# Performance work log

Hardware: AMD Instinct MI355X
Metric: run time of the kernel (lower is better)

Reference implementation:

```python
import jax, jax.numpy as jnp
import numpy as np

# dims
B, H, W = 2, 128, 256
MD = 34            # model_dim (last 2 channels = sin/cos lat)
LD = MD - 2        # learnable_dim = 32
NH, HD = 4, 8      # n_heads, head_dim
SH = 64            # shared_hidden (DISCO out channels)
K = 25             # number of DISCO basis functions (5x5 kernel_shape)
P = 7              # local stencil width (lat x lon support of geodesic basis)
R = P // 2
FF1, FF2 = 512, 256


def setup_inputs() -> dict:
    key = jax.random.key(0)
    ks = jax.random.split(key, 16)
    x = jax.random.normal(ks[0], (B, H, W, MD), dtype=jnp.float32)
    # latitude-dependent sparse geodesic basis values over a 7x7 stencil
    psi_val = jax.random.uniform(ks[1], (K, H, P * P), dtype=jnp.float32) * 0.1
    disco_w = jax.random.normal(ks[2], (SH, K), dtype=jnp.float32) * 0.1
    disco_b = jax.random.normal(ks[3], (SH,), dtype=jnp.float32) * 0.01
    # per-head MLP: shared_hidden -> 32 -> 1
    hw1 = jax.random.normal(ks[4], (NH, SH, 32), dtype=jnp.float32) * (1.0 / np.sqrt(SH))
    hb1 = jax.random.normal(ks[5], (NH, 32), dtype=jnp.float32) * 0.01
    hw2 = jax.random.normal(ks[6], (NH, 32, 1), dtype=jnp.float32) * (1.0 / np.sqrt(32))
    hb2 = jax.random.normal(ks[7], (NH, 1), dtype=jnp.float32) * 0.01
    # FFN: model_dim -> 512 -> 256 -> learnable_dim
    fw1 = jax.random.normal(ks[8], (MD, FF1), dtype=jnp.float32) * (1.0 / np.sqrt(MD))
    fw1 = fw1.at[-2:, :].set(0.0)  # matches ffn[0].weight[:, -2:] = 0 init
    fb1 = jax.random.normal(ks[9], (FF1,), dtype=jnp.float32) * 0.01
    fw2 = jax.random.normal(ks[10], (FF1, FF2), dtype=jnp.float32) * (1.0 / np.sqrt(FF1))
    fb2 = jax.random.normal(ks[11], (FF2,), dtype=jnp.float32) * 0.01
    fw3 = jax.random.normal(ks[12], (FF2, LD), dtype=jnp.float32) * (1.0 / np.sqrt(FF2))
    fb3 = jax.random.normal(ks[13], (LD,), dtype=jnp.float32) * 0.01
    return {"x": x, "psi_val": psi_val, "disco_w": disco_w, "disco_b": disco_b,
            "hw1": hw1, "hb1": hb1, "hw2": hw2, "hb2": hb2,
            "fw1": fw1, "fb1": fb1, "fw2": fw2, "fb2": fb2, "fw3": fw3, "fb3": fb3}


def _gelu(t):
    return jax.nn.gelu(t, approximate=False)  # torch nn.GELU default (erf)


def _disco_s2(xn, psi_val, disco_w, disco_b):
    """DISCO sparse-basis conv on single-channel maps.
    xn: (N, H, W). Basis values vary with output latitude, longitude is
    translation-invariant; support is a lat-clamped / lon-wrapped 7x7 stencil.
    Returns (N, SH, H, W)."""
    xp = jnp.pad(xn, ((0, 0), (R, R), (0, 0)), mode="edge")  # clamp at poles
    shifts = []
    for dlat in range(P):
        row = xp[:, dlat:dlat + H, :]
        for dlon in range(-R, R + 1):
            shifts.append(jnp.roll(row, -dlon, axis=2))  # wrap in longitude
    xs = jnp.stack(shifts, axis=1)  # (N, P*P, H, W)
    basis = jnp.einsum("khp,nphw->nkhw", psi_val, xs)       # basis aggregation
    return jnp.einsum("fk,nkhw->nfhw", disco_w, basis) + disco_b[None, :, None, None]


def reference(x, psi_val, disco_w, disco_b, hw1, hb1, hw2, hb2,
              fw1, fb1, fw2, fb2, fw3, fb3):
    x_learn = x[..., :LD]
    sin_cos = x[..., LD:]
    x_res = x_learn
    # (B,H,W,LD) -> (B*LD, H, W): each learnable channel is a 1-channel map
    xn = x_learn.transpose(0, 3, 1, 2).reshape(B * LD, H, W)
    d = _disco_s2(xn, psi_val, disco_w, disco_b)              # (B*LD, SH, H, W)
    d = d.reshape(B, LD, SH, H, W).transpose(0, 3, 4, 1, 2)    # (B,H,W,LD,SH)
    # per-head MLP over its head_dim slice (head index is outer in LD)
    d = d.reshape(B, H, W, NH, HD, SH)
    h = _gelu(jnp.einsum("bxynds,nso->bxyndo", d, hw1) + hb1[None, None, None, :, None, :])
    h = jnp.einsum("bxyndo,noe->bxynde", h, hw2) + hb2[None, None, None, :, None, :]
    x_learn = h[..., 0].reshape(B, H, W, LD)
    x_learn = x_learn + x_res                                  # use_residual
    x_full = jnp.concatenate([x_learn, sin_cos], axis=-1)
    x_res2 = x_learn
    t = _gelu(x_full @ fw1 + fb1)
    t = _gelu(t @ fw2 + fb2)
    t = t @ fw3 + fb3                                          # dropout p=0 -> id
    x_learn = t + x_res2
    return jnp.concatenate([x_learn, sin_cos], axis=-1)
```

## Files before the change

kernel.cpp:

```cpp
#include <hip/hip_runtime.h>
#include <math.h>


typedef __attribute__((ext_vector_type(8))) short bfrag;
typedef __attribute__((ext_vector_type(4))) float ffrag;
typedef __attribute__((ext_vector_type(4))) short short4v;

union bfi4 { int4 i; bfrag b; };

__device__ __forceinline__ float gelu_f(float v) {
  const float z = v * (2.3022077484f + 0.1029451564f * v * v);
  const float e = __builtin_amdgcn_exp2f(-z);
  return v * __builtin_amdgcn_rcpf(1.0f + e);
}

__device__ __forceinline__ short f2bf(float f) {
  union { float f; unsigned u; } v; v.f = f;
  unsigned r = (v.u + 0x7fffu + ((v.u >> 16) & 1u)) >> 16;
  return (short)r;
}

__device__ __forceinline__ short f2bf_fast(float f) {
  union { float f; unsigned u; } v; v.f = f;
  return (short)((v.u + 0x8000u) >> 16);
}

__device__ __forceinline__ float bf2f(short s) {
  union { float f; unsigned u; } v;
  v.u = ((unsigned)(unsigned short)s) << 16;
  return v.f;
}

template <int CTRL>
__device__ __forceinline__ float dpp_add(float v) {
  union { float f; int i; } s, t;
  s.f = v;
  t.i = __builtin_amdgcn_update_dpp(0, s.i, CTRL, 0xf, 0xf, true);
  return v + t.f;
}
__device__ __forceinline__ float reduce16(float v) {
  v = dpp_add<0xB1>(v);
  v = dpp_add<0x4E>(v);
  v = dpp_add<0x141>(v);
  v = dpp_add<0x140>(v);
  return v;
}

__device__ __forceinline__ void st4bf(short* p, float4 v) {
  short4v s;
  s[0] = f2bf(v.x); s[1] = f2bf(v.y); s[2] = f2bf(v.z); s[3] = f2bf(v.w);
  *(short4v*)p = s;
}

__global__ __launch_bounds__(256) void k01_prep(
    const float* __restrict__ psi, const float* __restrict__ dw,
    const float* __restrict__ db,
    const float* __restrict__ fw1, const float* __restrict__ fw2,
    const float* __restrict__ fw3, const float* __restrict__ hw1,
    const float* __restrict__ hb1,
    short* __restrict__ wcb, short* __restrict__ fw1s,
    short* __restrict__ fw2s, short* __restrict__ fw3s,
    float* __restrict__ hb1e) {
  __shared__ __align__(16) char sm[24832];
  const int bid = blockIdx.x;
  const int tid = threadIdx.x;

  if (bid < 512) {
    float* tileL = (float*)sm;
    float* hw1n  = (float*)(sm + 13312);
    short* tile2 = (short*)(sm + 21504);
    const int h = bid >> 2;
    const int n = bid & 3;
    const int lane = tid & 63;
    const int w = __builtin_amdgcn_readfirstlane(tid >> 6);

    for (int e = tid; e < 512; e += 256)
      ((float4*)hw1n)[e] = ((const float4*)(hw1 + n * 2048))[e];

    float dwreg[25];
#pragma unroll
    for (int kk = 0; kk < 25; ++kk) dwreg[kk] = dw[lane * 25 + kk];
    const int p0 = w * 13;
    const int pend = (p0 + 13 < 49) ? (p0 + 13) : 49;
#pragma unroll 1
    for (int p = p0; p < pend; ++p) {
      float acc = 0.f;
#pragma unroll
      for (int kk = 0; kk < 25; ++kk)
        acc += dwreg[kk] * psi[kk * 6272 + h * 49 + p];
      tileL[lane * 52 + p] = acc;
    }
    __syncthreads();

    const int o = tid & 31;
#pragma unroll 1
    for (int pp = tid >> 5; pp < 25; pp += 8) {
      const int p2 = pp * 2;
      float a0 = 0.f, a1 = 0.f;
#pragma unroll 4
      for (int f = 0; f < 64; ++f) {
        const float wv = hw1n[f * 32 + o];
        a0 += wv * tileL[f * 52 + p2];
        a1 += wv * tileL[f * 52 + p2 + 1];
      }
      tile2[o * 52 + p2] = f2bf(a0);
      if (p2 + 1 < 49) tile2[o * 52 + p2 + 1] = f2bf(a1);
    }
    __syncthreads();

    short* outp = wcb + h * 16384 + n * 4096;
    for (int idx = tid; idx < 4096; idx += 256) {
      const int jj = idx & 7, ln = (idx >> 3) & 63;
      const int nt = (idx >> 9) & 1, kt = (idx >> 10) & 1;
      const int par = idx >> 11;
      const int k = kt * 32 + ((ln >> 4) << 3) + jj;
      const int oo = nt * 16 + (ln & 15);
      const int r = k >> 3, dlt = k & 7;
      const int j = par ? (dlt - 1) : dlt;
      short v = 0;
      if (r < 7 && j >= 0 && j < 7) v = tile2[oo * 52 + r * 7 + j];
      outp[idx] = v;
    }
    return;
  }

  if (bid < 528) {
    short* S = (short*)sm;
    const int kt = bid - 512;
    const float* src = fw2 + kt * 8192;
    for (int q = tid; q < 2048; q += 256) {
      const int lin = q * 4;
      const int kk = lin >> 8, nn = lin & 255;
      st4bf(S + kk * 260 + nn, *(const float4*)(src + lin));
    }
    __syncthreads();
    short* dst = fw2s + kt * 8192;
    for (int q = tid; q < 8192; q += 256) {
      const int jj = q & 7, lane = (q >> 3) & 63, nt = q >> 9;
      const int kk = (lane >> 4) * 8 + jj, nn = nt * 16 + (lane & 15);
      dst[q] = S[kk * 260 + nn];
    }
    return;
  }

  if (bid < 530) {
    const int X = bid - 528;
    short* S = (short*)sm;
    for (int q = tid; q < 2048; q += 256) {
      const int lin = q * 4;
      const int kk = lin >> 8, nn = lin & 255;
      st4bf(S + kk * 260 + nn, *(const float4*)(fw1 + kk * 512 + X * 256 + nn));
    }
    __syncthreads();
    for (int q = tid; q < 8192; q += 256) {
      const int jj = q & 7, lane = (q >> 3) & 63, ntl = q >> 9;
      const int kk = (lane >> 4) * 8 + jj, nn = ntl * 16 + (lane & 15);
      fw1s[X * 8192 + q] = S[kk * 260 + nn];
    }
    return;
  }

  if (bid == 530) {
    short* S = (short*)sm;
    for (int q = tid; q < 2048; q += 256) {
      const int lin = q * 4;
      const int kk = lin >> 5, nn = lin & 31;
      st4bf(S + kk * 36 + nn, *(const float4*)(fw3 + lin));
    }
    __syncthreads();
    for (int q = tid; q < 8192; q += 256) {
      const int jj = q & 7, lane = (q >> 3) & 63;
      const int nt = (q >> 9) & 1, kt = q >> 10;
      const int kk = kt * 32 + (lane >> 4) * 8 + jj, nn = nt * 16 + (lane & 15);
      fw3s[q] = S[kk * 36 + nn];
    }
    return;
  }

  if (tid < 128) {
    const int n = tid >> 5, o = tid & 31;
    float acc = hb1[n * 32 + o];
#pragma unroll
    for (int s = 0; s < 64; ++s)
      acc += hw1[n * 2048 + s * 32 + o] * db[s];
    hb1e[tid] = acc;
  }
}

__global__ __launch_bounds__(256, 7) void k23_fused(
    const float* __restrict__ x,    const short* __restrict__ wcb,
    const float* __restrict__ hb1e, const float* __restrict__ hw2,
    const float* __restrict__ hb2,
    const short* __restrict__ fw1s, const short* __restrict__ fw2s,
    const short* __restrict__ fw3s,
    const float* __restrict__ fb1,  const float* __restrict__ fb2,
    const float* __restrict__ fb3,  float* __restrict__ outb) {
  __shared__ __align__(16) char smem[20256];
  short* sX = (short*)smem;
  short* sM = (short*)(smem + 18080);
  float* sO = (float*)smem;

  const int tid = threadIdx.x;

  const int lin  = blockIdx.x + (blockIdx.y << 3) + (blockIdx.z << 10);
  const int xcd  = lin & 7;
  const int slot = lin >> 3;
  const int w0   = (slot & 7) * 32;
  const int b    = (slot >> 3) & 1;
  const int h    = (xcd << 4) | (slot >> 4);

  const int lane = tid & 63, lm = lane & 15, lq = lane >> 4;
  const int n = tid >> 6;

  float hb1v[2], hw2v[2];
#pragma unroll
  for (int nt = 0; nt < 2; ++nt) {
    hb1v[nt] = hb1e[n * 32 + nt * 16 + lm];
    hw2v[nt] = hw2[n * 32 + nt * 16 + lm];
  }
  const float hb2n = hb2[n];

  {
    int4* p = (int4*)smem;
    int4 z; z.x = z.y = z.z = z.w = 0;
    for (int e = tid; e < 20256 / 16; e += 256) p[e] = z;
  }
  __syncthreads();

#pragma unroll 1
  for (int r = 0; r < 7; ++r) {
    int hr = h - 3 + r; hr = hr < 0 ? 0 : (hr > 127 ? 127 : hr);
    const float* __restrict__ xrow = x + (size_t)((b * 128 + hr) * 256) * 34;
    short* __restrict__ sxr = sX + r * 40;
    for (int e = tid; e < 39 * 16; e += 256) {
      const int c2 = e & 15;
      const int wp = e >> 4;
      const int wr = (w0 - 3 + wp) & 255;
      const float2 v = *(const float2*)&xrow[wr * 34 + c2 * 2];
      short* dp = sxr + (c2 * 2) * 280 + wp;
      dp[0]   = f2bf_fast(v.x);
      dp[280] = f2bf_fast(v.y);
    }
  }
  __syncthreads();

  const int* tpB = (const int*)sX;

#pragma unroll 1
  for (int par = 0; par < 2; ++par) {
    bfrag cw[2][2];
#pragma unroll
    for (int kt = 0; kt < 2; ++kt)
#pragma unroll
      for (int nt = 0; nt < 2; ++nt)
        cw[kt][nt] = *(const bfrag*)(wcb + h * 16384 + n * 4096 +
                         ((par * 2 + kt) * 2 + nt) * 512 + lane * 8);

#pragma unroll 1
    for (int i = 0; i < 8; ++i) {
      const int c = n * 8 + i;

      const int base0 = c * 140 + lq * 20 + lm;
      bfi4 u0, u1;
      u0.i.x = tpB[base0];      u0.i.y = tpB[base0 + 1];
      u0.i.z = tpB[base0 + 2];  u0.i.w = tpB[base0 + 3];
      u1.i.x = tpB[base0 + 80]; u1.i.y = tpB[base0 + 81];
      u1.i.z = tpB[base0 + 82]; u1.i.w = tpB[base0 + 83];

      ffrag h0 = {0.f, 0.f, 0.f, 0.f}, h1 = {0.f, 0.f, 0.f, 0.f};
      h0 = __builtin_amdgcn_mfma_f32_16x16x32_bf16(u0.b, cw[0][0], h0, 0, 0, 0);
      h0 = __builtin_amdgcn_mfma_f32_16x16x32_bf16(u1.b, cw[1][0], h0, 0, 0, 0);
      h1 = __builtin_amdgcn_mfma_f32_16x16x32_bf16(u0.b, cw[0][1], h1, 0, 0, 0);
      h1 = __builtin_amdgcn_mfma_f32_16x16x32_bf16(u1.b, cw[1][1], h1, 0, 0, 0);

#pragma unroll
      for (int rr = 0; rr < 4; ++rr) {
        float v = gelu_f(h0[rr] + hb1v[0]) * hw2v[0] +
                  gelu_f(h1[rr] + hb1v[1]) * hw2v[1];
        v = reduce16(v);
        const int p = 2 * (lq * 4 + rr) + par;
        const float res = bf2f(sX[c * 280 + 123 + p]);
        if (lm == 0) sM[p * 34 + c] = f2bf_fast(v + hb2n + res);
      }
    }
  }
  __syncthreads();

  short* sT1h = (short*)smem;
  short* sT2  = (short*)smem;
  const int wave = n;
  const int koff = lq * 8;
  const int mt3 = wave & 1;
  const int nt3 = wave >> 1;
  const int col3 = nt3 * 16 + lm;
  const int pixg = (b * 128 + h) * 256 + w0;

  const int n0 = wave * 4;
  ffrag acc[2][4];
#pragma unroll
  for (int mt = 0; mt < 2; ++mt)
#pragma unroll
    for (int ni = 0; ni < 4; ++ni) acc[mt][ni] = ffrag{0.f, 0.f, 0.f, 0.f};
  const short* w2base = fw2s + n0 * 512 + lane * 8;

#pragma unroll 1
  for (int H = 0; H < 2; ++H) {
    bfrag aF[2];
#pragma unroll
    for (int mt = 0; mt < 2; ++mt)
      aF[mt] = *(const bfrag*)(sM + (mt * 16 + lm) * 34 + koff);
#pragma unroll
    for (int ni = 0; ni < 4; ++ni) {
      const bfrag b1f = *(const bfrag*)(fw1s +
                          (H * 16 + wave * 4 + ni) * 512 + lane * 8);
      const int ntl = wave * 4 + ni;
#pragma unroll
      for (int mt = 0; mt < 2; ++mt) {
        ffrag cc = {0.f, 0.f, 0.f, 0.f};
        cc = __builtin_amdgcn_mfma_f32_16x16x32_bf16(aF[mt], b1f, cc, 0, 0, 0);
        const int colg = H * 256 + ntl * 16 + lm;
        const float bias = fb1[colg];
#pragma unroll
        for (int r = 0; r < 4; ++r) {
          const int row = mt * 16 + lq * 4 + r;
          sT1h[row * 264 + ntl * 16 + lm] = f2bf_fast(gelu_f(cc[r] + bias));
        }
      }
    }
    __syncthreads();

#pragma unroll 2
    for (int kt = 0; kt < 8; ++kt) {
      bfrag bv[4];
#pragma unroll
      for (int ni = 0; ni < 4; ++ni)
        bv[ni] = *(const bfrag*)(w2base + (H * 8 + kt) * 8192 + ni * 512);
      const bfrag a0 = *(const bfrag*)(sT1h + lm * 264 + kt * 32 + koff);
      const bfrag a1 = *(const bfrag*)(sT1h + (16 + lm) * 264 + kt * 32 + koff);
#pragma unroll
      for (int ni = 0; ni < 4; ++ni) {
        acc[0][ni] = __builtin_amdgcn_mfma_f32_16x16x32_bf16(a0, bv[ni], acc[0][ni], 0, 0, 0);
        acc[1][ni] = __builtin_amdgcn_mfma_f32_16x16x32_bf16(a1, bv[ni], acc[1][ni], 0, 0, 0);
      }
    }
    __syncthreads();
  }

#pragma unroll
  for (int mt = 0; mt < 2; ++mt)
#pragma unroll
    for (int ni = 0; ni < 4; ++ni) {
      const int col = (n0 + ni) * 16 + lm;
      const float bias = fb2[col];
#pragma unroll
      for (int r = 0; r < 4; ++r) {
        const int row = mt * 16 + lq * 4 + r;
        sT2[row * 264 + col] = f2bf_fast(gelu_f(acc[mt][ni][r] + bias));
      }
    }
  __syncthreads();

  ffrag c3 = {0.f, 0.f, 0.f, 0.f};
  const short* sA3 = sT2 + (mt3 * 16 + lm) * 264 + koff;
#pragma unroll
  for (int kt = 0; kt < 8; ++kt) {
    const bfrag a = *(const bfrag*)(sA3 + kt * 32);
    const bfrag bw = *(const bfrag*)(fw3s + nt3 * 512 + kt * 1024 + lane * 8);
    c3 = __builtin_amdgcn_mfma_f32_16x16x32_bf16(a, bw, c3, 0, 0, 0);
  }
  __syncthreads();
  {
    const float bias = fb3[col3];
#pragma unroll
    for (int r = 0; r < 4; ++r) {
      const int row = mt3 * 16 + lq * 4 + r;
      const float res = bf2f(sM[(mt3 * 16 + lq * 4 + r) * 34 + col3]);
      sO[row * 34 + col3] = c3[r] + bias + res;
    }
  }
  if (tid < 32) {
    const float2 scv =
        *(const float2*)&x[(size_t)(((b * 128 + h) * 256 + w0 + tid)) * 34 + 32];
    sO[tid * 34 + 32] = scv.x;
    sO[tid * 34 + 33] = scv.y;
  }
  __syncthreads();
  {
    const float4* sp = (const float4*)sO;
    float4* dp = (float4*)(outb + (size_t)pixg * 34);
    for (int e = tid; e < 272; e += 256) dp[e] = sp[e];
  }
}

extern "C" void kernel_launch(void* const* d_in, const int* in_sizes, int n_in,
                              void* d_out, int out_size, void* d_ws, size_t ws_size,
                              hipStream_t stream) {
  const float* x   = (const float*)d_in[0];
  const float* psi = (const float*)d_in[1];
  const float* dw  = (const float*)d_in[2];
  const float* db  = (const float*)d_in[3];
  const float* hw1 = (const float*)d_in[4];
  const float* hb1 = (const float*)d_in[5];
  const float* hw2 = (const float*)d_in[6];
  const float* hb2 = (const float*)d_in[7];
  const float* fw1 = (const float*)d_in[8];
  const float* fb1 = (const float*)d_in[9];
  const float* fw2 = (const float*)d_in[10];
  const float* fb2 = (const float*)d_in[11];
  const float* fw3 = (const float*)d_in[12];
  const float* fb3 = (const float*)d_in[13];
  float* outb = (float*)d_out;

  short* wcb  = (short*)d_ws;
  short* fw1s = wcb + 2097152;
  short* fw2s = fw1s + 16384;
  short* fw3s = fw2s + 131072;
  float* hb1e = (float*)(fw3s + 8192);

  hipLaunchKernelGGL(k01_prep, dim3(532), dim3(256), 0, stream,
                     psi, dw, db, fw1, fw2, fw3, hw1, hb1,
                     wcb, fw1s, fw2s, fw3s, hb1e);
  hipLaunchKernelGGL(k23_fused, dim3(8, 128, 2), dim3(256), 0, stream,
                     x, wcb, hb1e, hw2, hb2,
                     fw1s, fw2s, fw3s, fb1, fb2, fb3, outb);
}
```

Before: 169.1 us.

## Split fused DISCO conv and FFN kernel into two kernels via workspace

Splits the single fused kernel into a DISCO-conv/head-MLP kernel and an FFN kernel. The two share a bf16 intermediate tile of 32x32 per block written to a global workspace. Each kernel now targets 8 waves-per-SIMD occupancy instead of 7, and the FFN's second-layer loop is restructured to load fewer weight fragments at a time to cut register pressure. In exchange it adds an extra kernel launch, a global write and read of the intermediate, and a padded row stride of 36.

```diff
diff --git a/kernel.cpp b/kernel.cpp
--- a/kernel.cpp
+++ b/kernel.cpp
@@ -50,6 +50,15 @@
   short4v s;
   s[0] = f2bf(v.x); s[1] = f2bf(v.y); s[2] = f2bf(v.z); s[3] = f2bf(v.w);
   *(short4v*)p = s;
+}
+
+__device__ __forceinline__ void tile_map(int& w0, int& b, int& h, int& lin) {
+  lin  = blockIdx.x + (blockIdx.y << 3) + (blockIdx.z << 10);
+  const int xcd  = lin & 7;
+  const int slot = lin >> 3;
+  w0 = (slot & 7) * 32;
+  b  = (slot >> 3) & 1;
+  h  = (xcd << 4) | (slot >> 4);
 }
 
 __global__ __launch_bounds__(256) void k01_prep(
@@ -187,27 +196,17 @@
   }
 }
 
-__global__ __launch_bounds__(256, 7) void k23_fused(
+__global__ __launch_bounds__(256, 8) void k2_conv(
     const float* __restrict__ x,    const short* __restrict__ wcb,
     const float* __restrict__ hb1e, const float* __restrict__ hw2,
-    const float* __restrict__ hb2,
-    const short* __restrict__ fw1s, const short* __restrict__ fw2s,
-    const short* __restrict__ fw3s,
-    const float* __restrict__ fb1,  const float* __restrict__ fb2,
-    const float* __restrict__ fb3,  float* __restrict__ outb) {
-  __shared__ __align__(16) char smem[20256];
+    const float* __restrict__ hb2,  short* __restrict__ wsM) {
+  __shared__ __align__(16) char smem[20384];
   short* sX = (short*)smem;
   short* sM = (short*)(smem + 18080);
-  float* sO = (float*)smem;
 
   const int tid = threadIdx.x;
-
-  const int lin  = blockIdx.x + (blockIdx.y << 3) + (blockIdx.z << 10);
-  const int xcd  = lin & 7;
-  const int slot = lin >> 3;
-  const int w0   = (slot & 7) * 32;
-  const int b    = (slot >> 3) & 1;
-  const int h    = (xcd << 4) | (slot >> 4);
+  int w0, b, h, lin;
+  tile_map(w0, b, h, lin);
 
   const int lane = tid & 63, lm = lane & 15, lq = lane >> 4;
   const int n = tid >> 6;
@@ -223,7 +222,7 @@
   {
     int4* p = (int4*)smem;
     int4 z; z.x = z.y = z.z = z.w = 0;
-    for (int e = tid; e < 20256 / 16; e += 256) p[e] = z;
+    for (int e = tid; e < 20384 / 16; e += 256) p[e] = z;
   }
   __syncthreads();
 
@@ -280,22 +279,50 @@
         v = reduce16(v);
         const int p = 2 * (lq * 4 + rr) + par;
         const float res = bf2f(sX[c * 280 + 123 + p]);
-        if (lm == 0) sM[p * 34 + c] = f2bf_fast(v + hb2n + res);
+        if (lm == 0) sM[p * 36 + c] = f2bf_fast(v + hb2n + res);
       }
     }
   }
   __syncthreads();
 
+  {
+    const int row = tid >> 3, c4 = (tid & 7) * 4;
+    *(short4v*)(wsM + lin * 1024 + tid * 4) = *(const short4v*)(sM + row * 36 + c4);
+  }
+}
+
+__global__ __launch_bounds__(256, 8) void k3_mlp(
+    const float* __restrict__ x,    const short* __restrict__ wsM,
+    const short* __restrict__ fw1s, const short* __restrict__ fw2s,
+    const short* __restrict__ fw3s,
+    const float* __restrict__ fb1,  const float* __restrict__ fb2,
+    const float* __restrict__ fb3,  float* __restrict__ outb) {
+  __shared__ __align__(16) char smem[19200];
   short* sT1h = (short*)smem;
   short* sT2  = (short*)smem;
-  const int wave = n;
+  float* sO   = (float*)smem;
+  short* sMv  = (short*)(smem + 16896);
+
+  const int tid = threadIdx.x;
+  int w0, b, h, lin;
+  tile_map(w0, b, h, lin);
+
+  const int lane = tid & 63, lm = lane & 15, lq = lane >> 4;
+  const int wave = tid >> 6;
   const int koff = lq * 8;
+
+  {
+    const int row = tid >> 3, c4 = (tid & 7) * 4;
+    *(short4v*)(sMv + row * 36 + c4) = *(const short4v*)(wsM + lin * 1024 + tid * 4);
+  }
+  __syncthreads();
+
   const int mt3 = wave & 1;
   const int nt3 = wave >> 1;
   const int col3 = nt3 * 16 + lm;
   const int pixg = (b * 128 + h) * 256 + w0;
-
   const int n0 = wave * 4;
+
   ffrag acc[2][4];
 #pragma unroll
   for (int mt = 0; mt < 2; ++mt)
@@ -305,10 +332,6 @@
 
 #pragma unroll 1
   for (int H = 0; H < 2; ++H) {
-    bfrag aF[2];
-#pragma unroll
-    for (int mt = 0; mt < 2; ++mt)
-      aF[mt] = *(const bfrag*)(sM + (mt * 16 + lm) * 34 + koff);
 #pragma unroll
     for (int ni = 0; ni < 4; ++ni) {
       const bfrag b1f = *(const bfrag*)(fw1s +
@@ -316,10 +339,10 @@
       const int ntl = wave * 4 + ni;
 #pragma unroll
       for (int mt = 0; mt < 2; ++mt) {
+        const bfrag aFm = *(const bfrag*)(sMv + (mt * 16 + lm) * 36 + koff);
         ffrag cc = {0.f, 0.f, 0.f, 0.f};
-        cc = __builtin_amdgcn_mfma_f32_16x16x32_bf16(aF[mt], b1f, cc, 0, 0, 0);
-        const int colg = H * 256 + ntl * 16 + lm;
-        const float bias = fb1[colg];
+        cc = __builtin_amdgcn_mfma_f32_16x16x32_bf16(aFm, b1f, cc, 0, 0, 0);
+        const float bias = fb1[H * 256 + ntl * 16 + lm];
 #pragma unroll
         for (int r = 0; r < 4; ++r) {
           const int row = mt * 16 + lq * 4 + r;
@@ -329,18 +352,18 @@
     }
     __syncthreads();
 
-#pragma unroll 2
+#pragma unroll 1
     for (int kt = 0; kt < 8; ++kt) {
-      bfrag bv[4];
-#pragma unroll
-      for (int ni = 0; ni < 4; ++ni)
-        bv[ni] = *(const bfrag*)(w2base + (H * 8 + kt) * 8192 + ni * 512);
       const bfrag a0 = *(const bfrag*)(sT1h + lm * 264 + kt * 32 + koff);
       const bfrag a1 = *(const bfrag*)(sT1h + (16 + lm) * 264 + kt * 32 + koff);
 #pragma unroll
-      for (int ni = 0; ni < 4; ++ni) {
-        acc[0][ni] = __builtin_amdgcn_mfma_f32_16x16x32_bf16(a0, bv[ni], acc[0][ni], 0, 0, 0);
-        acc[1][ni] = __builtin_amdgcn_mfma_f32_16x16x32_bf16(a1, bv[ni], acc[1][ni], 0, 0, 0);
+      for (int np = 0; np < 2; ++np) {
+        const bfrag bv0 = *(const bfrag*)(w2base + (H * 8 + kt) * 8192 + (2 * np) * 512);
+        const bfrag bv1 = *(const bfrag*)(w2base + (H * 8 + kt) * 8192 + (2 * np + 1) * 512);
+        acc[0][2 * np]     = __builtin_amdgcn_mfma_f32_16x16x32_bf16(a0, bv0, acc[0][2 * np], 0, 0, 0);
+        acc[1][2 * np]     = __builtin_amdgcn_mfma_f32_16x16x32_bf16(a1, bv0, acc[1][2 * np], 0, 0, 0);
+        acc[0][2 * np + 1] = __builtin_amdgcn_mfma_f32_16x16x32_bf16(a0, bv1, acc[0][2 * np + 1], 0, 0, 0);
+        acc[1][2 * np + 1] = __builtin_amdgcn_mfma_f32_16x16x32_bf16(a1, bv1, acc[1][2 * np + 1], 0, 0, 0);
       }
     }
     __syncthreads();
@@ -374,7 +397,7 @@
 #pragma unroll
     for (int r = 0; r < 4; ++r) {
       const int row = mt3 * 16 + lq * 4 + r;
-      const float res = bf2f(sM[(mt3 * 16 + lq * 4 + r) * 34 + col3]);
+      const float res = bf2f(sMv[row * 36 + col3]);
       sO[row * 34 + col3] = c3[r] + bias + res;
     }
   }
@@ -416,11 +439,13 @@
   short* fw2s = fw1s + 16384;
   short* fw3s = fw2s + 131072;
   float* hb1e = (float*)(fw3s + 8192);
+  short* wsM  = (short*)(hb1e + 128);
 
   hipLaunchKernelGGL(k01_prep, dim3(532), dim3(256), 0, stream,
                      psi, dw, db, fw1, fw2, fw3, hw1, hb1,
                      wcb, fw1s, fw2s, fw3s, hb1e);
-  hipLaunchKernelGGL(k23_fused, dim3(8, 128, 2), dim3(256), 0, stream,
-                     x, wcb, hb1e, hw2, hb2,
-                     fw1s, fw2s, fw3s, fb1, fb2, fb3, outb);
-}
+  hipLaunchKernelGGL(k2_conv, dim3(8, 128, 2), dim3(256), 0, stream,
+                     x, wcb, hb1e, hw2, hb2, wsM);
+  hipLaunchKernelGGL(k3_mlp, dim3(8, 128, 2), dim3(256), 0, stream,
+                     x, wsM, fw1s, fw2s, fw3s, fb1, fb2, fb3, outb);
+}
```

Result: no change. 168.8 us (-0.2%).
